# Kernel optimization log

Measured on AMD Instinct MI355X. Metric: run time of the kernel, lower is better.

The kernel has to match this reference:

```python
import jax, jax.numpy as jnp
import numpy as np


def setup_inputs() -> dict:
    key = jax.random.key(0)
    kq, ks, kr, kx, ky = jax.random.split(key, 5)
    B, C, H, W, K = 2, 64, 128, 256, 32
    Q = jax.random.normal(kq, (B, C, H, W), dtype=jnp.float32)
    S = jax.random.normal(ks, (B, C, H, W), dtype=jnp.float32)
    R = jax.random.normal(kr, (B, C, H, W), dtype=jnp.float32)
    Pos_x = jax.random.randint(kx, (H * W, K), 0, H, dtype=jnp.int64 if jax.config.jax_enable_x64 else jnp.int32)
    Pos_y = jax.random.randint(ky, (H * W, K), 0, W, dtype=jnp.int64 if jax.config.jax_enable_x64 else jnp.int32)
    return {"Q": Q, "S": S, "R": R, "Pos_x": Pos_x, "Pos_y": Pos_y}


def reference(Q, S, R, Pos_x, Pos_y):
    B, C, H, W = Q.shape
    N = H * W
    px = Pos_x.reshape(-1)  # [N*K]
    py = Pos_y.reshape(-1)
    K = px.shape[0] // N
    # Gather keys/values at candidate positions: [B, C, N*K] -> [B, C, N, K]
    Key = S[:, :, px, py].reshape(B, C, N, K)
    Value = R[:, :, px, py].reshape(B, C, N, K)
    # Queries: [B, N, C]
    Qf = Q.reshape(B, C, N).transpose(0, 2, 1)
    # Per-pixel scores over K candidates (NO 1/sqrt(d) scaling, as in original)
    score = jnp.einsum('bnc,bcnk->bnk', Qf, Key)
    attn = jax.nn.softmax(score, axis=-1)
    # Attention-weighted sum of values: [B, N, C]
    out = jnp.einsum('bnk,bcnk->bnc', attn, Value)
    return out.reshape(B, H, W, C).transpose(0, 3, 1, 2)
```

## Files before the change

kernel.cpp:

```cpp
#include <hip/hip_runtime.h>
#include <hip/hip_fp16.h>

constexpr int B = 2, C = 64, H = 128, W = 256, N = H * W, K = 32;

__global__ __launch_bounds__(256) void transpose_cn_nc_h(
    const float* __restrict__ S, const float* __restrict__ R,
    __half* __restrict__ St, __half* __restrict__ Rt) {
    __shared__ float tile[C][65];
    const int n0 = blockIdx.x * 64;
    const int b  = blockIdx.y;
    const float* src = (blockIdx.z == 0 ? S : R) + (size_t)b * C * N;
    __half*      dst = (blockIdx.z == 0 ? St : Rt) + (size_t)b * N * C;

    {
        const int j = threadIdx.x & 63, c0 = threadIdx.x >> 6;
        const float* s = src + n0 + j;
#pragma unroll
        for (int r = 0; r < 16; ++r) {
            int c = c0 + r * 4;
            tile[c][j] = s[(size_t)c * N];
        }
    }
    __syncthreads();
    {
        const int c2 = threadIdx.x & 31;
        const int j0 = threadIdx.x >> 5;
        __half2* d2 = (__half2*)dst;
#pragma unroll
        for (int r = 0; r < 8; ++r) {
            int j = j0 + 8 * r;
            d2[(size_t)(n0 + j) * (C / 2) + c2] =
                __floats2half2_rn(tile[2 * c2][j], tile[2 * c2 + 1][j]);
        }
    }
}

__global__ __launch_bounds__(512) void fepam_attn(
    const float* __restrict__ Q,
    const int*   __restrict__ Px, const int* __restrict__ Py,
    const __half* __restrict__ St, const __half* __restrict__ Rt,
    float* __restrict__ Out) {
    __shared__ float qt[64][68];
    __shared__ float ot[64][65];

    const int tid  = threadIdx.x;
    const int lane = tid & 63;
    const int wave = tid >> 6;
    const int b    = blockIdx.y;
    const int n0   = blockIdx.x * 64;

    {
        const int j = tid & 63, c0 = tid >> 6;
        const float* qsrc = Q + (size_t)b * C * N + n0 + j;
#pragma unroll
        for (int r = 0; r < 8; ++r) {
            int c = c0 + r * 8;
            qt[j][c] = qsrc[(size_t)c * N];
        }
    }
    __syncthreads();

    const int k = lane & 31;
    const int h = lane >> 5;
    const __half* Stb = St + (size_t)b * N * C;
    const __half* Rtb = Rt + (size_t)b * N * C;

#pragma unroll 2
    for (int p = 0; p < 8; ++p) {
        const int j = wave * 8 + p;
        const int n = n0 + j;

        const int px  = Px[(size_t)n * K + k];
        const int py  = Py[(size_t)n * K + k];
        const int idx = px * W + py;

        const float4* kp = (const float4*)(Stb + (size_t)idx * C + h * 32);
        const float4* qp = (const float4*)(&qt[j][h * 32]);
        float s = 0.f;
#pragma unroll
        for (int i = 0; i < 4; ++i) {
            float4 kraw = kp[i];
            const __half2* k2 = (const __half2*)&kraw;
            float4 q0 = qp[2 * i], q1 = qp[2 * i + 1];
            float2 f0 = __half22float2(k2[0]);
            float2 f1 = __half22float2(k2[1]);
            float2 f2 = __half22float2(k2[2]);
            float2 f3 = __half22float2(k2[3]);
            s += q0.x * f0.x + q0.y * f0.y + q0.z * f1.x + q0.w * f1.y
               + q1.x * f2.x + q1.y * f2.y + q1.z * f3.x + q1.w * f3.y;
        }
        s += __shfl_xor(s, 32);

        float m = s;
#pragma unroll
        for (int mask = 16; mask >= 1; mask >>= 1)
            m = fmaxf(m, __shfl_xor(m, mask));
        float e = __expf(s - m);
        float l = e;
#pragma unroll
        for (int mask = 16; mask >= 1; mask >>= 1)
            l += __shfl_xor(l, mask);
        const float a = e / l;

        const int c2 = lane & 31;
        const int kh = lane >> 5;
        float accx = 0.f, accy = 0.f;
#pragma unroll
        for (int kk = 0; kk < 16; ++kk) {
            const int   srck = 2 * kk + kh;
            const int   idxk = __shfl(idx, srck);
            const float ak   = __shfl(a, srck);
            const __half2 v  = *(const __half2*)(Rtb + (size_t)idxk * C + 2 * c2);
            const float2 vf  = __half22float2(v);
            accx += ak * vf.x;
            accy += ak * vf.y;
        }
        accx += __shfl_xor(accx, 32);
        accy += __shfl_xor(accy, 32);
        if (lane < 32) {
            ot[j][2 * c2]     = accx;
            ot[j][2 * c2 + 1] = accy;
        }
    }
    __syncthreads();

    {
        const int j = tid & 63, c0 = tid >> 6;
        float* od = Out + (size_t)b * C * N + n0 + j;
#pragma unroll
        for (int r = 0; r < 8; ++r) {
            int c = c0 + r * 8;
            od[(size_t)c * N] = ot[j][c];
        }
    }
}

extern "C" void kernel_launch(void* const* d_in, const int* in_sizes, int n_in,
                              void* d_out, int out_size, void* d_ws, size_t ws_size,
                              hipStream_t stream) {
    const float* Q  = (const float*)d_in[0];
    const float* S  = (const float*)d_in[1];
    const float* R  = (const float*)d_in[2];
    const int*   Px = (const int*)d_in[3];
    const int*   Py = (const int*)d_in[4];
    float* Out = (float*)d_out;

    __half* St = (__half*)d_ws;
    __half* Rt = St + (size_t)B * N * C;

    dim3 tgrid(N / 64, B, 2);
    transpose_cn_nc_h<<<tgrid, 256, 0, stream>>>(S, R, St, Rt);

    dim3 agrid(N / 64, B);
    fepam_attn<<<agrid, 512, 0, stream>>>(Q, Px, Py, St, Rt, Out);
}
```

Measured before the change: 149.8 us.

## Pre-transpose Q to fp16, use fdot2 and DPP reductions, split score/value phases

```diff
diff --git a/kernel.cpp b/kernel.cpp
--- a/kernel.cpp
+++ b/kernel.cpp
@@ -3,15 +3,26 @@
 
 constexpr int B = 2, C = 64, H = 128, W = 256, N = H * W, K = 32;
 
-__global__ __launch_bounds__(256) void transpose_cn_nc_h(
-    const float* __restrict__ S, const float* __restrict__ R,
-    __half* __restrict__ St, __half* __restrict__ Rt) {
+typedef _Float16 hf2 __attribute__((ext_vector_type(2)));
+
+template <int CTRL>
+__device__ __forceinline__ float dppf(float x) {
+    int i = __builtin_bit_cast(int, x);
+    int r = __builtin_amdgcn_update_dpp(i, i, CTRL, 0xF, 0xF, false);
+    return __builtin_bit_cast(float, r);
+}
+
+__global__ __launch_bounds__(256) void transpose_to_h(
+    const float* __restrict__ Q, const float* __restrict__ S,
+    const float* __restrict__ R,
+    __half* __restrict__ Qt, __half* __restrict__ St, __half* __restrict__ Rt) {
     __shared__ float tile[C][65];
     const int n0 = blockIdx.x * 64;
     const int b  = blockIdx.y;
-    const float* src = (blockIdx.z == 0 ? S : R) + (size_t)b * C * N;
-    __half*      dst = (blockIdx.z == 0 ? St : Rt) + (size_t)b * N * C;
-
+    const int z  = blockIdx.z;
+    const float* src = (z == 0 ? S : (z == 1 ? R : Q)) + (size_t)b * C * N;
+    __half2* d2 = (__half2*)((z == 0 ? St : (z == 1 ? Rt : Qt)) +
+                             (size_t)b * N * C);
     {
         const int j = threadIdx.x & 63, c0 = threadIdx.x >> 6;
         const float* s = src + n0 + j;
@@ -23,104 +34,105 @@
     }
     __syncthreads();
     {
-        const int c2 = threadIdx.x & 31;
-        const int j0 = threadIdx.x >> 5;
-        __half2* d2 = (__half2*)dst;
+        const int c2 = threadIdx.x & 31, j0 = threadIdx.x >> 5;
 #pragma unroll
         for (int r = 0; r < 8; ++r) {
             int j = j0 + 8 * r;
-            d2[(size_t)(n0 + j) * (C / 2) + c2] =
+            d2[(size_t)(n0 + j) * 32 + c2] =
                 __floats2half2_rn(tile[2 * c2][j], tile[2 * c2 + 1][j]);
         }
     }
 }
 
-__global__ __launch_bounds__(512) void fepam_attn(
-    const float* __restrict__ Q,
-    const int*   __restrict__ Px, const int* __restrict__ Py,
+__global__ __launch_bounds__(512, 8) void fepam_attn(
+    const __half* __restrict__ Qt,
+    const int* __restrict__ Px, const int* __restrict__ Py,
     const __half* __restrict__ St, const __half* __restrict__ Rt,
     float* __restrict__ Out) {
-    __shared__ float qt[64][68];
-    __shared__ float ot[64][65];
+    __shared__ __align__(16) float ot[64][66];
+    __shared__ __align__(16) unsigned aidx[8][8][32];
 
     const int tid  = threadIdx.x;
     const int lane = tid & 63;
     const int wave = tid >> 6;
-    const int b    = blockIdx.y;
-    const int n0   = blockIdx.x * 64;
+    const int bx   = blockIdx.x;
+    const int b    = bx & 1;
+    const int n0   = (bx >> 1) * 64;
 
-    {
-        const int j = tid & 63, c0 = tid >> 6;
-        const float* qsrc = Q + (size_t)b * C * N + n0 + j;
-#pragma unroll
-        for (int r = 0; r < 8; ++r) {
-            int c = c0 + r * 8;
-            qt[j][c] = qsrc[(size_t)c * N];
-        }
-    }
-    __syncthreads();
+    const __half* Qtb = Qt + (size_t)b * N * C;
+    const __half* Stb = St + (size_t)b * N * C;
+    const __half* Rtb = Rt + (size_t)b * N * C;
 
     const int k = lane & 31;
     const int h = lane >> 5;
-    const __half* Stb = St + (size_t)b * N * C;
-    const __half* Rtb = Rt + (size_t)b * N * C;
-
 #pragma unroll 2
     for (int p = 0; p < 8; ++p) {
-        const int j = wave * 8 + p;
-        const int n = n0 + j;
+        const int n = n0 + wave * 8 + p;
 
         const int px  = Px[(size_t)n * K + k];
         const int py  = Py[(size_t)n * K + k];
         const int idx = px * W + py;
 
         const float4* kp = (const float4*)(Stb + (size_t)idx * C + h * 32);
-        const float4* qp = (const float4*)(&qt[j][h * 32]);
+        const float4* qp = (const float4*)(Qtb + (size_t)n * C + h * 32);
         float s = 0.f;
 #pragma unroll
         for (int i = 0; i < 4; ++i) {
             float4 kraw = kp[i];
-            const __half2* k2 = (const __half2*)&kraw;
-            float4 q0 = qp[2 * i], q1 = qp[2 * i + 1];
-            float2 f0 = __half22float2(k2[0]);
-            float2 f1 = __half22float2(k2[1]);
-            float2 f2 = __half22float2(k2[2]);
-            float2 f3 = __half22float2(k2[3]);
-            s += q0.x * f0.x + q0.y * f0.y + q0.z * f1.x + q0.w * f1.y
-               + q1.x * f2.x + q1.y * f2.y + q1.z * f3.x + q1.w * f3.y;
+            float4 qraw = qp[i];
+            const hf2* k2 = (const hf2*)&kraw;
+            const hf2* q2 = (const hf2*)&qraw;
+#pragma unroll
+            for (int u = 0; u < 4; ++u)
+                s = __builtin_amdgcn_fdot2(k2[u], q2[u], s, false);
         }
         s += __shfl_xor(s, 32);
 
         float m = s;
-#pragma unroll
-        for (int mask = 16; mask >= 1; mask >>= 1)
-            m = fmaxf(m, __shfl_xor(m, mask));
+        m = fmaxf(m, dppf<0xB1>(m));
+        m = fmaxf(m, dppf<0x4E>(m));
+        m = fmaxf(m, dppf<0x141>(m));
+        m = fmaxf(m, dppf<0x140>(m));
+        m = fmaxf(m, __shfl_xor(m, 16));
         float e = __expf(s - m);
         float l = e;
-#pragma unroll
-        for (int mask = 16; mask >= 1; mask >>= 1)
-            l += __shfl_xor(l, mask);
+        l += dppf<0xB1>(l);
+        l += dppf<0x4E>(l);
+        l += dppf<0x141>(l);
+        l += dppf<0x140>(l);
+        l += __shfl_xor(l, 16);
         const float a = e / l;
 
-        const int c2 = lane & 31;
-        const int kh = lane >> 5;
+        if (lane < 32)
+            aidx[wave][p][k] = ((unsigned)idx << 16) |
+                               (unsigned)__half_as_ushort(__float2half_rn(a));
+    }
+
+    const int c2 = lane & 31;
+    const int kh = lane >> 5;
+    for (int p = 0; p < 8; ++p) {
+        const int j = wave * 8 + p;
         float accx = 0.f, accy = 0.f;
 #pragma unroll
-        for (int kk = 0; kk < 16; ++kk) {
-            const int   srck = 2 * kk + kh;
-            const int   idxk = __shfl(idx, srck);
-            const float ak   = __shfl(a, srck);
-            const __half2 v  = *(const __half2*)(Rtb + (size_t)idxk * C + 2 * c2);
-            const float2 vf  = __half22float2(v);
-            accx += ak * vf.x;
-            accy += ak * vf.y;
+        for (int g = 0; g < 8; ++g) {
+            const uint4 pk4 = *(const uint4*)&aidx[wave][p][4 * g];
+            const unsigned ua = kh ? pk4.z : pk4.x;
+            const unsigned ub = kh ? pk4.w : pk4.y;
+#pragma unroll
+            for (int t = 0; t < 2; ++t) {
+                const unsigned u = t ? ub : ua;
+                const float a = __half2float(__ushort_as_half((unsigned short)(u & 0xffffu)));
+                const __half2 v =
+                    *(const __half2*)(Rtb + ((size_t)(u >> 16) << 6) + 2 * c2);
+                const float2 vf = __half22float2(v);
+                accx = fmaf(a, vf.x, accx);
+                accy = fmaf(a, vf.y, accy);
+            }
         }
         accx += __shfl_xor(accx, 32);
         accy += __shfl_xor(accy, 32);
-        if (lane < 32) {
-            ot[j][2 * c2]     = accx;
-            ot[j][2 * c2 + 1] = accy;
-        }
+        if (lane < 32)
+            *(float2*)&ot[j][2 * c2] = make_float2(accx, accy);
     }
     __syncthreads();
 
@@ -147,10 +159,11 @@
 
     __half* St = (__half*)d_ws;
     __half* Rt = St + (size_t)B * N * C;
+    __half* Qt = Rt + (size_t)B * N * C;
 
-    dim3 tgrid(N / 64, B, 2);
-    transpose_cn_nc_h<<<tgrid, 256, 0, stream>>>(S, R, St, Rt);
+    dim3 tgrid(N / 64, B, 3);
+    transpose_to_h<<<tgrid, 256, 0, stream>>>(Q, S, R, Qt, St, Rt);
 
-    dim3 agrid(N / 64, B);
-    fepam_attn<<<agrid, 512, 0, stream>>>(Q, Px, Py, St, Rt, Out);
+    dim3 agrid(N / 64 * B);
+    fepam_attn<<<agrid, 512, 0, stream>>>(Qt, Px, Py, St, Rt, Out);
 }
```

Result: slower. 154.2 us (+2.9%).
